# Kernel optimization log

Hardware: AMD Instinct MI355X
Metric: run time of the kernel (lower is better)

## Reference

```python
import jax, jax.numpy as jnp
import numpy as np

C = 1.0          # ball curvature (Manifold default)
EPS = 1e-7
MIN_NORM = 1e-15

def _artanh(x):
    return jnp.arctanh(jnp.clip(x, -1.0 + EPS, 1.0 - EPS))

def _expmap0(u):
    # exp map at origin of the Poincare ball
    n = jnp.clip(jnp.linalg.norm(u, axis=-1, keepdims=True), MIN_NORM, None)
    sc = np.sqrt(C).astype(np.float32)
    return jnp.tanh(sc * n) * u / (sc * n)

def _mobius_add(x, y):
    x2 = jnp.sum(x * x, axis=-1, keepdims=True)
    y2 = jnp.sum(y * y, axis=-1, keepdims=True)
    xy = jnp.sum(x * y, axis=-1, keepdims=True)
    num = (1.0 + 2.0 * C * xy + C * y2) * x + (1.0 - C * x2) * y
    den = 1.0 + 2.0 * C * xy + C * C * x2 * y2
    return num / jnp.clip(den, MIN_NORM, None)

def setup_inputs() -> dict:
    key = jax.random.key(0)
    k1, k2, k3, k4 = jax.random.split(key, 4)
    N, D, U = 8192, 256, 128
    features = jax.random.normal(k1, (N, D), jnp.float32) * 0.1
    adj = jax.random.randint(k2, (N, N), 0, 2, jnp.int32)
    kernel = jax.random.normal(k3, (D, U), jnp.float32) * (1.0 / np.sqrt(D)).astype(np.float32)
    bias = jax.random.normal(k4, (U,), jnp.float32) * 0.01
    return {"features": features, "adj": adj, "kernel": kernel, "bias": bias}

def reference(features, adj, kernel, bias):
    sc = np.sqrt(C).astype(np.float32)
    # dense matmul then lift to the ball
    x = _expmap0(features @ kernel)                     # [N, U]
    # pairwise hyperbolic distance via closed form of ||mobius_add(-x_i, x_j)||
    x2 = jnp.sum(x * x, axis=-1)                        # [N]
    xy = x @ x.T                                        # [N, N]
    A = 1.0 - 2.0 * C * xy + C * x2[None, :]            # [N, N]
    B = (1.0 - C * x2)[:, None]                         # [N, 1]
    num_sq = A * A * x2[:, None] - 2.0 * A * B * xy + B * B * x2[None, :]
    den = 1.0 - 2.0 * C * xy + C * C * x2[:, None] * x2[None, :]
    mnorm = jnp.sqrt(jnp.clip(num_sq, 0.0, None)) / jnp.clip(den, MIN_NORM, None)
    dist = (2.0 / sc) * _artanh(sc * mnorm)             # sqdist ** 0.5 == distance, [N, N]
    # adjacency-masked softmax (zeros -> -inf, as in tf.where(a != 0, a, float.min))
    a = dist * adj.astype(dist.dtype)
    a = jnp.where(a != 0, a, jnp.finfo(a.dtype).min)
    att = jax.nn.softmax(a, axis=-1)                    # [N, N]
    # mobius_matvec with exchange=True: hyperbolic analogue of att @ x (row-wise norm rescale)
    mx = att @ x                                        # [N, U]
    x_n = jnp.clip(jnp.sqrt(x2)[:, None], MIN_NORM, None)
    mx_n = jnp.clip(jnp.linalg.norm(mx, axis=-1, keepdims=True), MIN_NORM, None)
    out = jnp.tanh(mx_n / x_n * _artanh(sc * x_n)) * mx / (sc * mx_n)
    # hyperbolic bias
    b = _expmap0(bias[None, :])                         # [1, U]
    return _mobius_add(out, b)
```

## Files before the change

### kernel.cpp

```cpp
#include <hip/hip_runtime.h>
#include <hip/hip_bf16.h>
#include <math.h>

#define Nn 8192
#define Dd 256
#define Uu 128
#define MI 16
#define NJC 16
#define JCL (Nn / NJC)
#define TJ 32
#define NIT (JCL / TJ)

typedef __attribute__((ext_vector_type(4))) float f32x4;
typedef __attribute__((ext_vector_type(8))) short s16x8;
typedef __attribute__((ext_vector_type(4))) short s16x4;

#define MFMA_K32(a, b, c) __builtin_amdgcn_mfma_f32_16x16x32_bf16((a), (b), (c), 0, 0, 0)

#define GL_LDS(src, dst)                                                              \
  __builtin_amdgcn_global_load_lds(                                                   \
      (const __attribute__((address_space(1))) unsigned int*)(src),                   \
      (__attribute__((address_space(3))) unsigned int*)(dst), 16, 0, 0)

__device__ __forceinline__ f32x4 mfma_k16(s16x4 a, s16x4 b, f32x4 c){
#if __has_builtin(__builtin_amdgcn_mfma_f32_16x16x16bf16_1k)
  return __builtin_amdgcn_mfma_f32_16x16x16bf16_1k(a, b, c, 0, 0, 0);
#else
  asm("v_mfma_f32_16x16x16_bf16 %0, %1, %2, %0" : "+v"(c) : "v"(a), "v"(b));
  return c;
#endif
}

__device__ __forceinline__ short f2bf(float f){
  unsigned int u = __float_as_uint(f);
  u += 0x7fffu + ((u >> 16) & 1u);
  return (short)(u >> 16);
}

__device__ __forceinline__ float waveSum(float v){
  #pragma unroll
  for (int off = 32; off >= 1; off >>= 1) v += __shfl_xor(v, off);
  return v;
}

__global__ __launch_bounds__(256) void k_prep(const float* __restrict__ feat,
                                              const float* __restrict__ kern,
                                              const float* __restrict__ bias,
                                              short* __restrict__ xh,
                                              short* __restrict__ v4,
                                              float* __restrict__ x2,
                                              float* __restrict__ bb){
  const int t = threadIdx.x;
  const int u = t & 127;
  const int g = t >> 7;
  const int n0 = blockIdx.x * 16;
  __shared__ float fS[16][Dd];
  __shared__ float red[4][8];
  __shared__ float redb[4];
  {
    const f32x4* fg = (const f32x4*)(feat + (size_t)n0 * Dd);
    f32x4* fd = (f32x4*)fS;
    #pragma unroll
    for (int c = 0; c < 4; ++c) fd[c * 256 + t] = fg[c * 256 + t];
  }
  __syncthreads();
  float zz[8];
  #pragma unroll
  for (int r = 0; r < 8; ++r) zz[r] = 0.f;
  for (int dq = 0; dq < 64; ++dq){
    const int d = dq * 4;
    const float k0 = kern[(size_t)(d + 0) * Uu + u];
    const float k1 = kern[(size_t)(d + 1) * Uu + u];
    const float k2 = kern[(size_t)(d + 2) * Uu + u];
    const float k3 = kern[(size_t)(d + 3) * Uu + u];
    #pragma unroll
    for (int r = 0; r < 8; ++r){
      const f32x4 f4 = *(const f32x4*)&fS[g * 8 + r][d];
      zz[r] = fmaf(f4.x, k0, fmaf(f4.y, k1, fmaf(f4.z, k2, fmaf(f4.w, k3, zz[r]))));
    }
  }
  #pragma unroll
  for (int r = 0; r < 8; ++r){
    float v = waveSum(zz[r] * zz[r]);
    if ((t & 63) == 0) red[t >> 6][r] = v;
  }
  __syncthreads();
  float scl[8];
  #pragma unroll
  for (int r = 0; r < 8; ++r){
    const float ns  = (g == 0) ? (red[0][r] + red[1][r]) : (red[2][r] + red[3][r]);
    const float nrm = fmaxf(sqrtf(ns), 1e-15f);
    const float th  = tanhf(nrm);
    scl[r] = th / nrm;
    xh[(size_t)(n0 + g * 8 + r) * Uu + u] = f2bf(zz[r] * scl[r]);
  }
  {
    short* vt = v4 + (size_t)blockIdx.x * 2048 + (size_t)(u >> 4) * 256 + (u & 15) * 4;
    #pragma unroll
    for (int qq = 0; qq < 2; ++qq){
      s16x4 w;
      #pragma unroll
      for (int e = 0; e < 4; ++e) w[e] = f2bf(zz[qq * 4 + e] * scl[qq * 4 + e]);
      *(s16x4*)(vt + (g * 2 + qq) * 64) = w;
    }
  }
  if (t < 16){
    const float ns  = (t < 8) ? (red[0][t] + red[1][t]) : (red[2][t - 8] + red[3][t - 8]);
    const float nrm = fmaxf(sqrtf(ns), 1e-15f);
    const float th  = tanhf(nrm);
    x2[n0 + t] = th * th;
  }
  if (blockIdx.x == 0){
    const float bv = (t < 128) ? bias[t] : 0.f;
    float v = waveSum(bv * bv);
    if ((t & 63) == 0) redb[t >> 6] = v;
    __syncthreads();
    const float n2  = redb[0] + redb[1] + redb[2] + redb[3];
    const float nrm = fmaxf(sqrtf(n2), 1e-15f);
    const float th  = tanhf(nrm);
    if (t < 128) bb[t] = bv * th / nrm;
    if (t == 0) bb[Uu] = th * th;
  }
}

__global__ __launch_bounds__(256, 2) void k_attn(const int* __restrict__ adj,
                                                 const short* __restrict__ xh,
                                                 const short* __restrict__ v4,
                                                 const float* __restrict__ x2g,
                                                 float* __restrict__ Opart,
                                                 float* __restrict__ lpart){
  const int t    = threadIdx.x;
  const int lane = t & 63;
  const int wid  = t >> 6;
  const int l15  = lane & 15;
  const int q4   = lane >> 4;
  const int ig   = blockIdx.x >> 4;
  const int jc   = blockIdx.x & 15;
  const int i0   = ig * 128 + wid * 32;
  const int jbase = jc * JCL;

  __shared__ __align__(16) short kb[2][4096];
  __shared__ __align__(16) short vb[2][4096];
  __shared__ __align__(16) float x2S[JCL];

  const char* ksrcW = (const char*)xh + (size_t)jbase * 256
                      + l15 * 256 + wid * 64 + q4 * 16;
  const char* vsrcW = (const char*)v4 + (size_t)(jbase >> 4) * 4096
                      + wid * 1024 + lane * 16;

  GL_LDS(ksrcW,        (char*)&kb[0][0] + wid * 1024);
  GL_LDS(ksrcW + 4096, (char*)&kb[0][0] + 4096 + wid * 1024);
  GL_LDS(vsrcW,        (char*)&vb[0][0] + wid * 1024);
  GL_LDS(vsrcW + 4096, (char*)&vb[0][0] + 4096 + wid * 1024);
  if (wid < 2)
    GL_LDS((const char*)(x2g + jbase) + wid * 1024 + lane * 16, (char*)x2S + wid * 1024);

  s16x8 qf[2][4];
  float x2i[2], Bv2j[2], nBv2[2];
  int   itDiag[2], sDiag[2];
  #pragma unroll
  for (int g = 0; g < 2; ++g){
    const int irow = i0 + g * 16 + l15;
    const short* qp = xh + (size_t)irow * Uu + q4 * 8;
    #pragma unroll
    for (int kk = 0; kk < 4; ++kk) qf[g][kk] = *(const s16x8*)(qp + kk * 32);
    const float xi = x2g[irow];
    x2i[g]  = xi;
    const float Bv = 1.f - xi;
    Bv2j[g] = Bv * Bv;
    nBv2[g] = -2.f * Bv;
    const int i0g = i0 + g * 16;
    itDiag[g] = ((i0g >> 9) == jc) ? ((i0g & 511) >> 5) : -1;
    sDiag[g]  = (i0g >> 4) & 1;
  }

  f32x4 oc[2][8];
  #pragma unroll
  for (int g = 0; g < 2; ++g)
    #pragma unroll
    for (int uc = 0; uc < 8; ++uc) oc[g][uc] = (f32x4){0.f, 0.f, 0.f, 0.f};
  float lacc[2] = {0.f, 0.f};

  const int* ap0 = adj + (size_t)(i0 + l15) * Nn + jbase + q4 * 4;
  const int* ap1 = adj + (size_t)(i0 + 16 + l15) * Nn + jbase + q4 * 4;
  int4 aqC[4];
  aqC[0] = *(const int4*)(ap0);
  aqC[1] = *(const int4*)(ap0 + 16);
  aqC[2] = *(const int4*)(ap1);
  aqC[3] = *(const int4*)(ap1 + 16);

  asm volatile("s_waitcnt vmcnt(0)" ::: "memory");
  __builtin_amdgcn_s_barrier();
  __builtin_amdgcn_sched_barrier(0);

  #pragma unroll 1
  for (int it = 0; it < NIT; ++it){
    const int cur = it & 1;
    if (it + 1 < NIT){
      const size_t o = (size_t)(it + 1) * 8192;
      GL_LDS(ksrcW + o,        (char*)&kb[cur ^ 1][0] + wid * 1024);
      GL_LDS(ksrcW + o + 4096, (char*)&kb[cur ^ 1][0] + 4096 + wid * 1024);
      GL_LDS(vsrcW + o,        (char*)&vb[cur ^ 1][0] + wid * 1024);
      GL_LDS(vsrcW + o + 4096, (char*)&vb[cur ^ 1][0] + 4096 + wid * 1024);
    }
    __builtin_amdgcn_sched_barrier(0);
    const int itn = (it + 1 < NIT) ? (it + 1) : (NIT - 1);
    int4 aqN[4];
    aqN[0] = *(const int4*)(ap0 + itn * 32);
    aqN[1] = *(const int4*)(ap0 + itn * 32 + 16);
    aqN[2] = *(const int4*)(ap1 + itn * 32);
    aqN[3] = *(const int4*)(ap1 + itn * 32 + 16);
    __builtin_amdgcn_sched_barrier(0);

    #pragma unroll
    for (int sdx = 0; sdx < 2; ++sdx){
      const char* kbp = (const char*)&kb[cur][0] + sdx * 4096;
      const char* vbp = (const char*)&vb[cur][0] + sdx * 4096;
      s16x8 kf[4];
      #pragma unroll
      for (int kk = 0; kk < 4; ++kk)
        kf[kk] = *(const s16x8*)(kbp + kk * 1024 + lane * 16);
      f32x4 s0 = {0.f, 0.f, 0.f, 0.f};
      f32x4 s1 = {0.f, 0.f, 0.f, 0.f};
      #pragma unroll
      for (int kk = 0; kk < 4; ++kk){
        s0 = MFMA_K32(kf[kk], qf[0][kk], s0);
        s1 = MFMA_K32(kf[kk], qf[1][kk], s1);
      }
      const f32x4 x2j = *(const f32x4*)&x2S[it * TJ + sdx * 16 + q4 * 4];
      s16x4 vf[8];
      #pragma unroll
      for (int uc = 0; uc < 8; ++uc)
        vf[uc] = *(const s16x4*)(vbp + uc * 512 + lane * 8);

      s16x4 pbg[2];
      #pragma unroll
      for (int g = 0; g < 2; ++g){
        const f32x4 sv = g ? s1 : s0;
        const int4  aq = aqC[g * 2 + sdx];
        const int aarr[4] = {aq.x, aq.y, aq.z, aq.w};
        float pv[4];
        #pragma unroll
        for (int r = 0; r < 4; ++r){
          const float xy  = sv[r];
          const float x2v = x2j[r];
          const float Aa  = fmaf(-2.f, xy, 1.f + x2v);
          const float num = fmaf(Aa * Aa, x2i[g], fmaf(nBv2[g] * Aa, xy, Bv2j[g] * x2v));
          const float den = fmaf(x2i[g], x2v, fmaf(-2.f, xy, 1.f));
          const float sq  = __builtin_amdgcn_sqrtf(fmaxf(num, 0.f));
          const float pd  = fmaxf(den - sq, 1e-30f);
          const float p   = fminf((den + sq) * __builtin_amdgcn_rcpf(pd), 2.0e7f);
          const bool keep = (aarr[r] != 0) && (sq != 0.f);
          pv[r] = keep ? p : 0.f;
        }
        if (it == itDiag[g] && sdx == sDiag[g]){
          const int j0 = jbase + it * TJ + sdx * 16;
          const int irow = i0 + g * 16 + l15;
          #pragma unroll
          for (int r = 0; r < 4; ++r)
            if ((j0 + 4 * q4 + r) == irow) pv[r] = 0.f;
        }
        lacc[g] += (pv[0] + pv[1]) + (pv[2] + pv[3]);
        s16x4 pb;
        #pragma unroll
        for (int r = 0; r < 4; ++r) pb[r] = f2bf(pv[r]);
        pbg[g] = pb;
      }

      #pragma unroll
      for (int uc = 0; uc < 8; ++uc){
        oc[0][uc] = mfma_k16(vf[uc], pbg[0], oc[0][uc]);
        oc[1][uc] = mfma_k16(vf[uc], pbg[1], oc[1][uc]);
      }
    }

    aqC[0] = aqN[0]; aqC[1] = aqN[1]; aqC[2] = aqN[2]; aqC[3] = aqN[3];
    asm volatile("s_waitcnt vmcnt(4)" ::: "memory");
    __builtin_amdgcn_s_barrier();
    __builtin_amdgcn_sched_barrier(0);
  }

  #pragma unroll
  for (int g = 0; g < 2; ++g){
    float la = lacc[g];
    la += __shfl_xor(la, 16);
    la += __shfl_xor(la, 32);
    if (lane < 16) lpart[(size_t)jc * Nn + i0 + g * 16 + lane] = la;
    float* op = Opart + ((size_t)jc * Nn + i0 + g * 16 + l15) * Uu + q4 * 4;
    #pragma unroll
    for (int uc = 0; uc < 8; ++uc) *(f32x4*)(op + uc * 16) = oc[g][uc];
  }
}

__global__ __launch_bounds__(256) void k_out(const float* __restrict__ Opart,
                                             const float* __restrict__ lpart,
                                             const float* __restrict__ x2g,
                                             const float* __restrict__ bb,
                                             float* __restrict__ out){
  const int t  = threadIdx.x;
  const int i0 = blockIdx.x * MI;
  const int er = t >> 4;
  const int ec = t & 15;
  float l = 0.f;
  #pragma unroll
  for (int c = 0; c < NJC; ++c) l += lpart[(size_t)c * Nn + i0 + er];
  const float linv = 1.f / fmaxf(l, 1e-30f);
  float mx[8]; float s2 = 0.f;
  #pragma unroll
  for (int k = 0; k < 8; ++k){
    float v = 0.f;
    #pragma unroll
    for (int c = 0; c < NJC; ++c)
      v += Opart[((size_t)c * Nn + i0 + er) * Uu + ec + 16 * k];
    v *= linv;
    mx[k] = v; s2 = fmaf(v, v, s2);
  }
  s2 += __shfl_xor(s2, 1); s2 += __shfl_xor(s2, 2);
  s2 += __shfl_xor(s2, 4); s2 += __shfl_xor(s2, 8);
  const float mx_n = fmaxf(sqrtf(s2), 1e-15f);
  const float x2e  = x2g[i0 + er];
  const float x_n  = fmaxf(sqrtf(x2e), 1e-15f);
  const float xcl  = fminf(x_n, 1.f - 1e-7f);
  const float art  = 0.5f * __logf((1.f + xcl) / (1.f - xcl));
  const float th   = tanhf(mx_n / x_n * art);
  const float rmn  = th / mx_n;
  float o[8], bu[8]; float ob = 0.f;
  #pragma unroll
  for (int k = 0; k < 8; ++k){
    bu[k] = bb[ec + 16 * k];
    o[k]  = mx[k] * rmn;
    ob = fmaf(o[k], bu[k], ob);
  }
  ob += __shfl_xor(ob, 1); ob += __shfl_xor(ob, 2);
  ob += __shfl_xor(ob, 4); ob += __shfl_xor(ob, 8);
  const float o2   = th * th;
  const float b2   = bb[Uu];
  const float cnum = 1.f + 2.f * ob + b2;
  const float cden = fmaf(o2, b2, 1.f + 2.f * ob);
  const float rden = 1.f / fmaxf(cden, 1e-15f);
  const float co   = 1.f - o2;
  #pragma unroll
  for (int k = 0; k < 8; ++k)
    out[(size_t)(i0 + er) * Uu + ec + 16 * k] = (cnum * o[k] + co * bu[k]) * rden;
}

extern "C" void kernel_launch(void* const* d_in, const int* in_sizes, int n_in,
                              void* d_out, int out_size, void* d_ws, size_t ws_size,
                              hipStream_t stream){
  (void)in_sizes; (void)n_in; (void)out_size; (void)ws_size;
  const float* feat = (const float*)d_in[0];
  const int*   adj  = (const int*)d_in[1];
  const float* kern = (const float*)d_in[2];
  const float* bias = (const float*)d_in[3];

  float* Opart = (float*)d_ws;
  float* lpart = Opart + (size_t)NJC * Nn * Uu;
  float* x2    = lpart + (size_t)NJC * Nn;
  float* bbw   = x2 + Nn;
  short* xh    = (short*)(bbw + 132);
  short* v4    = xh + (size_t)Nn * Uu;

  k_prep<<<Nn / 16, 256, 0, stream>>>(feat, kern, bias, xh, v4, x2, bbw);
  k_attn<<<(Nn / 128) * NJC, 256, 0, stream>>>(adj, xh, v4, x2, Opart, lpart);
  k_out <<<Nn / MI, 256, 0, stream>>>(Opart, lpart, x2, bbw, (float*)d_out);
}
```

Before: 445.9 us.

## Stage adjacency tiles through LDS and shrink j-tile to raise occupancy

The attention kernel now loads adjacency values with async global-to-LDS copies, double-buffered alongside the K/V tiles, instead of prefetching them into registers. The j-tile shrinks from 32 to 16 columns per iteration to fit LDS, and launch bounds go from 2 to 3 blocks per SIMD. The aim is to free registers and hide latency through higher occupancy. In exchange there are twice as many iterations and barriers, and the wait is now a full vmcnt(0) drain each step, which weakens the overlap between loads and compute.

```diff
diff --git a/kernel.cpp b/kernel.cpp
--- a/kernel.cpp
+++ b/kernel.cpp
@@ -8,8 +8,7 @@
 #define MI 16
 #define NJC 16
 #define JCL (Nn / NJC)
-#define TJ 32
-#define NIT (JCL / TJ)
+#define NIT (JCL / 16)
 
 typedef __attribute__((ext_vector_type(4))) float f32x4;
 typedef __attribute__((ext_vector_type(8))) short s16x8;
@@ -123,7 +122,7 @@
   }
 }
 
-__global__ __launch_bounds__(256, 2) void k_attn(const int* __restrict__ adj,
+__global__ __launch_bounds__(256, 3) void k_attn(const int* __restrict__ adj,
                                                  const short* __restrict__ xh,
                                                  const short* __restrict__ v4,
                                                  const float* __restrict__ x2g,
@@ -139,25 +138,27 @@
   const int i0   = ig * 128 + wid * 32;
   const int jbase = jc * JCL;
 
-  __shared__ __align__(16) short kb[2][4096];
-  __shared__ __align__(16) short vb[2][4096];
+  __shared__ __align__(16) short kb[2][2048];
+  __shared__ __align__(16) short vb[2][2048];
+  __shared__ __align__(16) int   ab[2][2048];
   __shared__ __align__(16) float x2S[JCL];
 
-  const char* ksrcW = (const char*)xh + (size_t)jbase * 256
-                      + l15 * 256 + wid * 64 + q4 * 16;
-  const char* vsrcW = (const char*)v4 + (size_t)(jbase >> 4) * 4096
-                      + wid * 1024 + lane * 16;
-
-  GL_LDS(ksrcW,        (char*)&kb[0][0] + wid * 1024);
-  GL_LDS(ksrcW + 4096, (char*)&kb[0][0] + 4096 + wid * 1024);
-  GL_LDS(vsrcW,        (char*)&vb[0][0] + wid * 1024);
-  GL_LDS(vsrcW + 4096, (char*)&vb[0][0] + 4096 + wid * 1024);
+  const char* ksrc = (const char*)xh + (size_t)jbase * 256
+                     + l15 * 256 + wid * 64 + q4 * 16;
+  const char* vsrc = (const char*)v4 + (size_t)jbase * 256 + wid * 1024 + lane * 16;
+  const char* asrc0 = (const char*)(adj + (size_t)(i0 + l15) * Nn + jbase + q4 * 4);
+  const char* asrc1 = (const char*)(adj + (size_t)(i0 + 16 + l15) * Nn + jbase + q4 * 4);
+
+  GL_LDS(ksrc,  (char*)&kb[0][0] + wid * 1024);
+  GL_LDS(vsrc,  (char*)&vb[0][0] + wid * 1024);
+  GL_LDS(asrc0, (char*)&ab[0][0] + wid * 2048);
+  GL_LDS(asrc1, (char*)&ab[0][0] + wid * 2048 + 1024);
   if (wid < 2)
     GL_LDS((const char*)(x2g + jbase) + wid * 1024 + lane * 16, (char*)x2S + wid * 1024);
 
   s16x8 qf[2][4];
   float x2i[2], Bv2j[2], nBv2[2];
-  int   itDiag[2], sDiag[2];
+  int   itDiag[2];
   #pragma unroll
   for (int g = 0; g < 2; ++g){
     const int irow = i0 + g * 16 + l15;
@@ -170,8 +171,7 @@
     Bv2j[g] = Bv * Bv;
     nBv2[g] = -2.f * Bv;
     const int i0g = i0 + g * 16;
-    itDiag[g] = ((i0g >> 9) == jc) ? ((i0g & 511) >> 5) : -1;
-    sDiag[g]  = (i0g >> 4) & 1;
+    itDiag[g] = ((i0g >> 9) == jc) ? ((i0g & 511) >> 4) : -1;
   }
 
   f32x4 oc[2][8];
@@ -180,14 +180,6 @@
     #pragma unroll
     for (int uc = 0; uc < 8; ++uc) oc[g][uc] = (f32x4){0.f, 0.f, 0.f, 0.f};
   float lacc[2] = {0.f, 0.f};
-
-  const int* ap0 = adj + (size_t)(i0 + l15) * Nn + jbase + q4 * 4;
-  const int* ap1 = adj + (size_t)(i0 + 16 + l15) * Nn + jbase + q4 * 4;
-  int4 aqC[4];
-  aqC[0] = *(const int4*)(ap0);
-  aqC[1] = *(const int4*)(ap0 + 16);
-  aqC[2] = *(const int4*)(ap1);
-  aqC[3] = *(const int4*)(ap1 + 16);
 
   asm volatile("s_waitcnt vmcnt(0)" ::: "memory");
   __builtin_amdgcn_s_barrier();
@@ -197,85 +189,75 @@
   for (int it = 0; it < NIT; ++it){
     const int cur = it & 1;
     if (it + 1 < NIT){
-      const size_t o = (size_t)(it + 1) * 8192;
-      GL_LDS(ksrcW + o,        (char*)&kb[cur ^ 1][0] + wid * 1024);
-      GL_LDS(ksrcW + o + 4096, (char*)&kb[cur ^ 1][0] + 4096 + wid * 1024);
-      GL_LDS(vsrcW + o,        (char*)&vb[cur ^ 1][0] + wid * 1024);
-      GL_LDS(vsrcW + o + 4096, (char*)&vb[cur ^ 1][0] + 4096 + wid * 1024);
+      const size_t o = (size_t)(it + 1) * 4096;
+      const size_t a = (size_t)(it + 1) * 64;
+      GL_LDS(ksrc + o,   (char*)&kb[cur ^ 1][0] + wid * 1024);
+      GL_LDS(vsrc + o,   (char*)&vb[cur ^ 1][0] + wid * 1024);
+      GL_LDS(asrc0 + a,  (char*)&ab[cur ^ 1][0] + wid * 2048);
+      GL_LDS(asrc1 + a,  (char*)&ab[cur ^ 1][0] + wid * 2048 + 1024);
     }
     __builtin_amdgcn_sched_barrier(0);
-    const int itn = (it + 1 < NIT) ? (it + 1) : (NIT - 1);
-    int4 aqN[4];
-    aqN[0] = *(const int4*)(ap0 + itn * 32);
-    aqN[1] = *(const int4*)(ap0 + itn * 32 + 16);
-    aqN[2] = *(const int4*)(ap1 + itn * 32);
-    aqN[3] = *(const int4*)(ap1 + itn * 32 + 16);
-    __builtin_amdgcn_sched_barrier(0);
-
-    #pragma unroll
-    for (int sdx = 0; sdx < 2; ++sdx){
-      const char* kbp = (const char*)&kb[cur][0] + sdx * 4096;
-      const char* vbp = (const char*)&vb[cur][0] + sdx * 4096;
-      s16x8 kf[4];
+
+    s16x8 kf[4];
+    #pragma unroll
+    for (int kk = 0; kk < 4; ++kk)
+      kf[kk] = *(const s16x8*)((const char*)&kb[cur][0] + kk * 1024 + lane * 16);
+    f32x4 s0 = {0.f, 0.f, 0.f, 0.f};
+    f32x4 s1 = {0.f, 0.f, 0.f, 0.f};
+    #pragma unroll
+    for (int kk = 0; kk < 4; ++kk){
+      s0 = MFMA_K32(kf[kk], qf[0][kk], s0);
+      s1 = MFMA_K32(kf[kk], qf[1][kk], s1);
+    }
+
+    s16x4 vf[8];
+    #pragma unroll
+    for (int uc = 0; uc < 8; ++uc)
+      vf[uc] = *(const s16x4*)((const char*)&vb[cur][0] + uc * 512 + lane * 8);
+    const f32x4 x2j = *(const f32x4*)&x2S[it * 16 + q4 * 4];
+
+    s16x4 pbg[2];
+    #pragma unroll
+    for (int g = 0; g < 2; ++g){
+      const int4 aq = *(const int4*)((const char*)&ab[cur][0]
+                                     + wid * 2048 + g * 1024 + lane * 16);
+      const f32x4 sv = g ? s1 : s0;
+      const int aarr[4] = {aq.x, aq.y, aq.z, aq.w};
+      float pv[4];
       #pragma unroll
-      for (int kk = 0; kk < 4; ++kk)
-        kf[kk] = *(const s16x8*)(kbp + kk * 1024 + lane * 16);
-      f32x4 s0 = {0.f, 0.f, 0.f, 0.f};
-      f32x4 s1 = {0.f, 0.f, 0.f, 0.f};
+      for (int r = 0; r < 4; ++r){
+        const float xy  = sv[r];
+        const float x2v = x2j[r];
+        const float Aa  = fmaf(-2.f, xy, 1.f + x2v);
+        const float num = fmaf(Aa * Aa, x2i[g], fmaf(nBv2[g] * Aa, xy, Bv2j[g] * x2v));
+        const float den = fmaf(x2i[g], x2v, fmaf(-2.f, xy, 1.f));
+        const float sq  = __builtin_amdgcn_sqrtf(fmaxf(num, 0.f));
+        const float pd  = fmaxf(den - sq, 1e-30f);
+        const float p   = fminf((den + sq) * __builtin_amdgcn_rcpf(pd), 2.0e7f);
+        const bool keep = (aarr[r] != 0) && (sq != 0.f);
+        pv[r] = keep ? p : 0.f;
+      }
+      if (it == itDiag[g]){
+        const int j0 = jbase + it * 16;
+        const int irow = i0 + g * 16 + l15;
+        #pragma unroll
+        for (int r = 0; r < 4; ++r)
+          if ((j0 + 4 * q4 + r) == irow) pv[r] = 0.f;
+      }
+      lacc[g] += (pv[0] + pv[1]) + (pv[2] + pv[3]);
+      s16x4 pb;
       #pragma unroll
-      for (int kk = 0; kk < 4; ++kk){
-        s0 = MFMA_K32(kf[kk], qf[0][kk], s0);
-        s1 = MFMA_K32(kf[kk], qf[1][kk], s1);
-      }
-      const f32x4 x2j = *(const f32x4*)&x2S[it * TJ + sdx * 16 + q4 * 4];
-      s16x4 vf[8];
-      #pragma unroll
-      for (int uc = 0; uc < 8; ++uc)
-        vf[uc] = *(const s16x4*)(vbp + uc * 512 + lane * 8);
-
-      s16x4 pbg[2];
-      #pragma unroll
-      for (int g = 0; g < 2; ++g){
-        const f32x4 sv = g ? s1 : s0;
-        const int4  aq = aqC[g * 2 + sdx];
-        const int aarr[4] = {aq.x, aq.y, aq.z, aq.w};
-        float pv[4];
-        #pragma unroll
-        for (int r = 0; r < 4; ++r){
-          const float xy  = sv[r];
-          const float x2v = x2j[r];
-          const float Aa  = fmaf(-2.f, xy, 1.f + x2v);
-          const float num = fmaf(Aa * Aa, x2i[g], fmaf(nBv2[g] * Aa, xy, Bv2j[g] * x2v));
-          const float den = fmaf(x2i[g], x2v, fmaf(-2.f, xy, 1.f));
-          const float sq  = __builtin_amdgcn_sqrtf(fmaxf(num, 0.f));
-          const float pd  = fmaxf(den - sq, 1e-30f);
-          const float p   = fminf((den + sq) * __builtin_amdgcn_rcpf(pd), 2.0e7f);
-          const bool keep = (aarr[r] != 0) && (sq != 0.f);
-          pv[r] = keep ? p : 0.f;
-        }
-        if (it == itDiag[g] && sdx == sDiag[g]){
-          const int j0 = jbase + it * TJ + sdx * 16;
-          const int irow = i0 + g * 16 + l15;
-          #pragma unroll
-          for (int r = 0; r < 4; ++r)
-            if ((j0 + 4 * q4 + r) == irow) pv[r] = 0.f;
-        }
-        lacc[g] += (pv[0] + pv[1]) + (pv[2] + pv[3]);
-        s16x4 pb;
-        #pragma unroll
-        for (int r = 0; r < 4; ++r) pb[r] = f2bf(pv[r]);
-        pbg[g] = pb;
-      }
-
-      #pragma unroll
-      for (int uc = 0; uc < 8; ++uc){
-        oc[0][uc] = mfma_k16(vf[uc], pbg[0], oc[0][uc]);
-        oc[1][uc] = mfma_k16(vf[uc], pbg[1], oc[1][uc]);
-      }
-    }
-
-    aqC[0] = aqN[0]; aqC[1] = aqN[1]; aqC[2] = aqN[2]; aqC[3] = aqN[3];
-    asm volatile("s_waitcnt vmcnt(4)" ::: "memory");
+      for (int r = 0; r < 4; ++r) pb[r] = f2bf(pv[r]);
+      pbg[g] = pb;
+    }
+
+    #pragma unroll
+    for (int uc = 0; uc < 8; ++uc){
+      oc[0][uc] = mfma_k16(vf[uc], pbg[0], oc[0][uc]);
+      oc[1][uc] = mfma_k16(vf[uc], pbg[1], oc[1][uc]);
+    }
+
+    asm volatile("s_waitcnt vmcnt(0)" ::: "memory");
     __builtin_amdgcn_s_barrier();
     __builtin_amdgcn_sched_barrier(0);
   }
```

Measured after the change: 476.2 us. +6.8%, slower.
